# Kernel optimization log

Measured on AMD Instinct MI355X. Metric: run time of the kernel, lower is better.

## Reference

```python
import jax, jax.numpy as jnp
import numpy as np

# AlphaPose skeleton (directed, as used by the module) -------------------
_EDGES = [(0,5),(0,6),(1,2),(2,4),(1,3),(5,7),(7,9),(6,8),(8,10),(5,6),
          (5,11),(6,12),(11,12),(11,13),(13,15),(12,14),(14,16)]
_N = 17

def _gcn_norm_adj():
    # PyG GCNConv: add self-loops, deg from target (col), norm = d^-1/2[src]*d^-1/2[dst]
    A = np.zeros((_N, _N), dtype=np.float32)
    for s, t in _EDGES:
        A[t, s] = 1.0               # message flows source -> target
    A += np.eye(_N, dtype=np.float32)  # self loops
    deg = A.sum(axis=1)                # in-degree incl. self loop
    dinv = 1.0 / np.sqrt(deg)
    return (dinv[:, None] * A * dinv[None, :]).astype(np.float32)

A_HAT = jnp.asarray(_gcn_norm_adj())  # [17,17], A_hat[t,s]

B, T, F, H, LH, C = 256, 128, 2, 128, 256, 1


def setup_inputs() -> dict:
    key = jax.random.key(0)
    ks = jax.random.split(key, 8)
    s = 0.05
    return {
        "keypoints": jax.random.normal(ks[0], (B, T, _N, F), jnp.float32),
        "W1": jax.random.normal(ks[1], (F, H), jnp.float32) * s,
        "b1": jnp.zeros((H,), jnp.float32),
        "W2": jax.random.normal(ks[2], (H, H), jnp.float32) * s,
        "b2": jnp.zeros((H,), jnp.float32),
        "W_ih": jax.random.normal(ks[3], (4 * LH, H), jnp.float32) * s,
        "W_hh": jax.random.normal(ks[4], (4 * LH, LH), jnp.float32) * s,
        "b_ih": jnp.zeros((4 * LH,), jnp.float32),
        "b_hh": jnp.zeros((4 * LH,), jnp.float32),
        "W_fc": jax.random.normal(ks[5], (C, LH), jnp.float32) * s,
        "b_fc": jnp.zeros((C,), jnp.float32),
    }


def _lstm(x, W_ih, W_hh, b_ih, b_hh):
    # x: [B, T, H] -> hs: [B, T, LH]; PyTorch gate order i, f, g, o
    b, lh = x.shape[0], W_hh.shape[1]
    bias = b_ih + b_hh
    xw = jnp.einsum('bth,gh->btg', x, W_ih) + bias  # precompute input proj

    def step(carry, xt):
        h, c = carry
        z = xt + h @ W_hh.T
        i, f, g, o = jnp.split(z, 4, axis=-1)
        i, f, o = jax.nn.sigmoid(i), jax.nn.sigmoid(f), jax.nn.sigmoid(o)
        g = jnp.tanh(g)
        c = f * c + i * g
        h = o * jnp.tanh(c)
        return (h, c), h

    h0 = jnp.zeros((b, lh), x.dtype)
    _, hs = jax.lax.scan(step, (h0, h0), xw.transpose(1, 0, 2))
    return hs.transpose(1, 0, 2)


def reference(keypoints, W1, b1, W2, b2, W_ih, W_hh, b_ih, b_hh, W_fc, b_fc):
    # Batched GCNConv: out = A_hat @ (X W) + b, fused over all B*T frames
    x = jnp.einsum('nm,btmh->btnh', A_HAT, keypoints @ W1) + b1
    x = jax.nn.relu(x)
    x = jnp.einsum('nm,btmh->btnh', A_HAT, x @ W2) + b2
    x = jax.nn.relu(x)
    pooled = x.mean(axis=2)                      # global_mean_pool -> [B,T,H]
    hs = _lstm(pooled, W_ih, W_hh, b_ih, b_hh)   # [B,T,LH]
    feat = hs.max(axis=1)                        # max over time -> [B,LH]
    out = feat @ W_fc.T + b_fc                   # [B,1]
    return jax.nn.sigmoid(out).squeeze(1)        # [B]
```

## Files before the change

### kernel.cpp

```cpp
#include <hip/hip_runtime.h>
#include <hip/hip_bf16.h>
#include <math.h>

#define NNODE 17
#define HF    128
#define TT    128
#define BB    256
#define LHID  256
#define G4    1024
#define ZSTR  1032

typedef short short8 __attribute__((ext_vector_type(8)));
typedef float f32x4  __attribute__((ext_vector_type(4)));

#define OFF_AHAT   0
#define OFF_WIT    512
#define OFF_BIAS   (OFF_WIT + 131072)
#define OFF_WPK    (OFF_BIAS + 1024)
#define OFF_POOLED (OFF_WPK + 131072)
#define OFF_XW     (OFF_POOLED + 4194304)
#define OFF_FEAT   (OFF_XW + 33554432)

__device__ inline unsigned int f2bf(float x) {
    unsigned int u = __float_as_uint(x);
    return (u + 0x7fffu + ((u >> 16) & 1u)) >> 16;
}

__global__ __launch_bounds__(64) void prep_ahat_k(float* __restrict__ Ahat) {
    __shared__ float A[289];
    __shared__ float dinv[NNODE];
    const int t = threadIdx.x;
    for (int i = t; i < 289; i += 64) A[i] = 0.f;
    __syncthreads();
    if (t == 0) {
        const int es[17] = {0,0,1,2,1,5,7,6,8,5,5,6,11,11,13,12,14};
        const int et[17] = {5,6,2,4,3,7,9,8,10,6,11,12,12,13,15,14,16};
        for (int e = 0; e < 17; e++) A[et[e]*17 + es[e]] = 1.f;
        for (int n = 0; n < NNODE; n++) A[n*17 + n] += 1.f;
    }
    __syncthreads();
    if (t < NNODE) {
        float s = 0.f;
        for (int m = 0; m < NNODE; m++) s += A[t*17 + m];
        dinv[t] = rsqrtf(s);
    }
    __syncthreads();
    for (int i = t; i < 289; i += 64) {
        int n = i / 17, m = i % 17;
        Ahat[i] = dinv[n] * A[i] * dinv[m];
    }
}

__global__ __launch_bounds__(256) void prep_wt_k(
    const float* __restrict__ Wih,
    const float* __restrict__ bih, const float* __restrict__ bhh,
    float* __restrict__ WIT, float* __restrict__ bias_sum)
{
    const int k = blockIdx.x;
    const int g0 = threadIdx.x;
    for (int g = g0; g < G4; g += 256)
        WIT[(size_t)k*G4 + g] = Wih[(size_t)g*HF + k];
    if (k == 0)
        for (int g = g0; g < G4; g += 256)
            bias_sum[g] = bih[g] + bhh[g];
}

__global__ __launch_bounds__(256) void prep_pack_k(
    const float* __restrict__ Whh, unsigned short* __restrict__ Wpk)
{
    const int tid = blockIdx.x * 256 + threadIdx.x;
    const int lane = tid & 63;
    const int kc   = (tid >> 6) & 7;
    const int t    = (tid >> 9) & 7;
    const int w    = (tid >> 12) & 7;
    const int col  = w*128 + t*16 + (lane & 15);
    const int kb   = kc*32 + (lane >> 4)*8;
    const float4 v0 = *(const float4*)(Whh + (size_t)col*LHID + kb);
    const float4 v1 = *(const float4*)(Whh + (size_t)col*LHID + kb + 4);
    uint4 o;
    o.x = f2bf(v0.x) | (f2bf(v0.y) << 16);
    o.y = f2bf(v0.z) | (f2bf(v0.w) << 16);
    o.z = f2bf(v1.x) | (f2bf(v1.y) << 16);
    o.w = f2bf(v1.z) | (f2bf(v1.w) << 16);
    *(uint4*)(Wpk + (size_t)tid*8) = o;
}

__global__ __launch_bounds__(128) void gcn_pool_k(
    const float* __restrict__ kp, const float* __restrict__ W1,
    const float* __restrict__ b1, const float* __restrict__ W2,
    const float* __restrict__ b2, const float* __restrict__ Ahat,
    float* __restrict__ pooled)
{
    const int f = blockIdx.x;
    const int j = threadIdx.x;
    __shared__ float Ah[289];
    __shared__ float X[34];
    __shared__ float AhT[128][20];
    if (j < 34) X[j] = kp[(size_t)f*34 + j];
    for (int i = j; i < 289; i += 128) Ah[i] = Ahat[i];
    __syncthreads();
    float ax0[NNODE], ax1[NNODE];
    #pragma unroll
    for (int n = 0; n < NNODE; n++) {
        float s0 = 0.f, s1 = 0.f;
        #pragma unroll
        for (int m = 0; m < NNODE; m++) {
            float a = Ah[n*17 + m];
            s0 += a * X[2*m];
            s1 += a * X[2*m + 1];
        }
        ax0[n] = s0; ax1[n] = s1;
    }
    const float w10 = W1[j], w11 = W1[HF + j], bb1 = b1[j];
    float h1[NNODE];
    #pragma unroll
    for (int n = 0; n < NNODE; n++)
        h1[n] = fmaxf(fmaf(ax0[n], w10, fmaf(ax1[n], w11, bb1)), 0.f);
    float gcol[NNODE];
    #pragma unroll
    for (int n = 0; n < NNODE; n++) {
        float s = 0.f;
        #pragma unroll
        for (int m = 0; m < NNODE; m++) s += Ah[n*17 + m] * h1[m];
        gcol[n] = s;
    }
    #pragma unroll
    for (int n = 0; n < NNODE; n++) AhT[j][n] = gcol[n];
    __syncthreads();
    float acc[NNODE];
    #pragma unroll
    for (int n = 0; n < NNODE; n++) acc[n] = 0.f;
    for (int k = 0; k < HF; k++) {
        float w = W2[k*HF + j];
        #pragma unroll
        for (int n = 0; n < NNODE; n++) acc[n] = fmaf(AhT[k][n], w, acc[n]);
    }
    const float bb2 = b2[j];
    float s = 0.f;
    #pragma unroll
    for (int n = 0; n < NNODE; n++) s += fmaxf(acc[n] + bb2, 0.f);
    pooled[(size_t)f*HF + j] = s * (1.f/17.f);
}

__global__ __launch_bounds__(256) void xw_gemm_k(
    const float* __restrict__ pooled, const float* __restrict__ WIT,
    const float* __restrict__ bias_sum, float* __restrict__ xw)
{
    const int row0 = blockIdx.x * 16;
    const int col  = blockIdx.y * 256 + threadIdx.x;
    __shared__ float P[16][HF];
    #pragma unroll
    for (int i = 0; i < 8; i++) {
        int e = threadIdx.x + i*256;
        P[e >> 7][e & 127] = pooled[(size_t)(row0 + (e >> 7))*HF + (e & 127)];
    }
    __syncthreads();
    float acc[16];
    #pragma unroll
    for (int r = 0; r < 16; r++) acc[r] = 0.f;
    for (int k = 0; k < HF; k++) {
        float w = WIT[(size_t)k*G4 + col];
        #pragma unroll
        for (int r = 0; r < 16; r++) acc[r] = fmaf(P[r][k], w, acc[r]);
    }
    float bs = bias_sum[col];
    #pragma unroll
    for (int r = 0; r < 16; r++)
        xw[(size_t)(row0 + r)*G4 + col] = acc[r] + bs;
}

__global__ __launch_bounds__(1024, 4) void lstm_mfma_k(
    const float* __restrict__ xw, const unsigned short* __restrict__ Wpk,
    float* __restrict__ feat)
{
    const int b0  = blockIdx.x * 8;
    const int tid = threadIdx.x;
    const int w   = tid >> 6;
    const int l   = tid & 63;
    const int kh  = w >> 3;
    const int cg  = w & 7;
    const int row = tid >> 7;
    const int u0  = (tid & 127) * 2;

    __shared__ float zbuf[2][8][ZSTR];
    __shared__ unsigned short hpack[8][64][8];

    if (tid < 512) ((uint4*)hpack)[tid] = make_uint4(0u, 0u, 0u, 0u);

    float c0 = 0.f, c1 = 0.f;
    float hm0 = -1e30f, hm1 = -1e30f;
    const unsigned short* wb = Wpk + (size_t)cg*32768 + (size_t)kh*2048 + (size_t)l*8;
    const float* xb = xw + ((size_t)(b0 + row)*TT)*G4 + u0;
    const int zr = (l >> 4) * 4;
    const int zc = cg*128 + (l & 15);
    __syncthreads();

    for (int t = 0; t < TT; ++t) {
        float2 xg[4];
        #pragma unroll
        for (int g = 0; g < 4; ++g)
            xg[g] = *(const float2*)(xb + (size_t)t*G4 + g*256);

        short8 a[4];
        #pragma unroll
        for (int kc = 0; kc < 4; ++kc)
            a[kc] = *(const short8*)&hpack[kh*4 + kc][l][0];

        short8 bc[4], bn[4];
        #pragma unroll
        for (int kc = 0; kc < 4; ++kc)
            bc[kc] = *(const short8*)(wb + kc*512);
        for (int tt = 0; tt < 8; ++tt) {
            if (tt < 7) {
                #pragma unroll
                for (int kc = 0; kc < 4; ++kc)
                    bn[kc] = *(const short8*)(wb + (tt+1)*4096 + kc*512);
            }
            f32x4 acc = {0.f, 0.f, 0.f, 0.f};
            #pragma unroll
            for (int kc = 0; kc < 4; ++kc)
                acc = __builtin_amdgcn_mfma_f32_16x16x32_bf16(a[kc], bc[kc], acc, 0, 0, 0);
            if (l < 32) {
                #pragma unroll
                for (int r = 0; r < 4; ++r)
                    zbuf[kh][zr + r][tt*16 + zc] = acc[r];
            }
            #pragma unroll
            for (int kc = 0; kc < 4; ++kc) bc[kc] = bn[kc];
        }
        __syncthreads();

        float2 ziA = *(const float2*)&zbuf[0][row][0*256 + u0];
        float2 ziB = *(const float2*)&zbuf[1][row][0*256 + u0];
        float2 zfA = *(const float2*)&zbuf[0][row][1*256 + u0];
        float2 zfB = *(const float2*)&zbuf[1][row][1*256 + u0];
        float2 zgA = *(const float2*)&zbuf[0][row][2*256 + u0];
        float2 zgB = *(const float2*)&zbuf[1][row][2*256 + u0];
        float2 zoA = *(const float2*)&zbuf[0][row][3*256 + u0];
        float2 zoB = *(const float2*)&zbuf[1][row][3*256 + u0];
        float hval[2];
        #pragma unroll
        for (int q = 0; q < 2; ++q) {
            float vi = ((const float*)&ziA)[q] + ((const float*)&ziB)[q] + ((const float*)&xg[0])[q];
            float vf = ((const float*)&zfA)[q] + ((const float*)&zfB)[q] + ((const float*)&xg[1])[q];
            float vg = ((const float*)&zgA)[q] + ((const float*)&zgB)[q] + ((const float*)&xg[2])[q];
            float vo = ((const float*)&zoA)[q] + ((const float*)&zoB)[q] + ((const float*)&xg[3])[q];
            float ii = __builtin_amdgcn_rcpf(1.f + __expf(-vi));
            float ff = __builtin_amdgcn_rcpf(1.f + __expf(-vf));
            float gg = 1.f - 2.f * __builtin_amdgcn_rcpf(__expf(2.f*vg) + 1.f);
            float oo = 1.f / (1.f + __expf(-vo));
            float cc = (q == 0) ? c0 : c1;
            float cn = fmaf(ff, cc, ii * gg);
            if (q == 0) c0 = cn; else c1 = cn;
            float th = 1.f - 2.f * __builtin_amdgcn_rcpf(__expf(2.f*cn) + 1.f);
            float hh = oo * th;
            if (q == 0) hm0 = fmaxf(hm0, hh); else hm1 = fmaxf(hm1, hh);
            hval[q] = hh;
        }
        unsigned int hp = f2bf(hval[0]) | (f2bf(hval[1]) << 16);
        *(unsigned int*)&hpack[u0 >> 5][((u0 >> 3) & 3)*16 + row][u0 & 7] = hp;
        __syncthreads();
    }
    *(float2*)(feat + (size_t)(b0 + row)*LHID + u0) = make_float2(hm0, hm1);
}

__global__ __launch_bounds__(64) void final_k(
    const float* __restrict__ feat, const float* __restrict__ Wfc,
    const float* __restrict__ bfc, float* __restrict__ out)
{
    const int b = blockIdx.x * 64 + threadIdx.x;
    float s = bfc[0];
    for (int u = 0; u < LHID; u++)
        s = fmaf(feat[(size_t)b*LHID + u], Wfc[u], s);
    out[b] = 1.f / (1.f + __expf(-s));
}

extern "C" void kernel_launch(void* const* d_in, const int* in_sizes, int n_in,
                              void* d_out, int out_size, void* d_ws, size_t ws_size,
                              hipStream_t stream) {
    const float* kp  = (const float*)d_in[0];
    const float* W1  = (const float*)d_in[1];
    const float* b1  = (const float*)d_in[2];
    const float* W2  = (const float*)d_in[3];
    const float* b2  = (const float*)d_in[4];
    const float* Wih = (const float*)d_in[5];
    const float* Whh = (const float*)d_in[6];
    const float* bih = (const float*)d_in[7];
    const float* bhh = (const float*)d_in[8];
    const float* Wfc = (const float*)d_in[9];
    const float* bfc = (const float*)d_in[10];

    float* ws     = (float*)d_ws;
    float* Ahat   = ws + OFF_AHAT;
    float* WIT    = ws + OFF_WIT;
    float* bias   = ws + OFF_BIAS;
    unsigned short* Wpk = (unsigned short*)(ws + OFF_WPK);
    float* pooled = ws + OFF_POOLED;
    float* xw     = ws + OFF_XW;
    float* feat   = ws + OFF_FEAT;
    float* out    = (float*)d_out;

    hipLaunchKernelGGL(prep_ahat_k, dim3(1), dim3(64), 0, stream, Ahat);
    hipLaunchKernelGGL(prep_wt_k, dim3(128), dim3(256), 0, stream,
                       Wih, bih, bhh, WIT, bias);
    hipLaunchKernelGGL(prep_pack_k, dim3(128), dim3(256), 0, stream, Whh, Wpk);
    hipLaunchKernelGGL(gcn_pool_k, dim3(BB*TT), dim3(128), 0, stream,
                       kp, W1, b1, W2, b2, Ahat, pooled);
    hipLaunchKernelGGL(xw_gemm_k, dim3(BB*TT/16, 4), dim3(256), 0, stream,
                       pooled, WIT, bias, xw);
    hipLaunchKernelGGL(lstm_mfma_k, dim3(BB/8), dim3(1024), 0, stream, xw, Wpk, feat);
    hipLaunchKernelGGL(final_k, dim3(4), dim3(64), 0, stream, feat, Wfc, bfc, out);
}
```

Measured before the change: 1.601 ms.

## Keep W_hh resident in registers across LSTM timesteps and drop K-split

Each wave now loads its 4x8 short8 slice of the packed W_hh once before the time loop and keeps it in registers. Previously those weights were re-streamed from global memory on every one of the 128 steps. The K dimension is no longer split across two wave halves, so each wave runs the full 8-chunk MFMA reduction for 4 column tiles. This removes the second zbuf partial-sum buffer and the extra adds. The cost is much higher register pressure (128 VGPRs for weights alone) with launch bounds of 1024 threads, so spills are possible.

```diff
diff --git a/kernel.cpp b/kernel.cpp
--- a/kernel.cpp
+++ b/kernel.cpp
@@ -177,22 +177,27 @@
     const int tid = threadIdx.x;
     const int w   = tid >> 6;
     const int l   = tid & 63;
-    const int kh  = w >> 3;
-    const int cg  = w & 7;
     const int row = tid >> 7;
     const int u0  = (tid & 127) * 2;
 
-    __shared__ float zbuf[2][8][ZSTR];
+    __shared__ float zbuf[8][ZSTR];
     __shared__ unsigned short hpack[8][64][8];
 
     if (tid < 512) ((uint4*)hpack)[tid] = make_uint4(0u, 0u, 0u, 0u);
+
+    const unsigned short* wb = Wpk + (size_t)(w >> 1)*32768 + (size_t)(w & 1)*16384 + (size_t)l*8;
+    short8 wreg[4][8];
+    #pragma unroll
+    for (int tt = 0; tt < 4; ++tt)
+        #pragma unroll
+        for (int kc = 0; kc < 8; ++kc)
+            wreg[tt][kc] = *(const short8*)(wb + tt*4096 + kc*512);
 
     float c0 = 0.f, c1 = 0.f;
     float hm0 = -1e30f, hm1 = -1e30f;
-    const unsigned short* wb = Wpk + (size_t)cg*32768 + (size_t)kh*2048 + (size_t)l*8;
     const float* xb = xw + ((size_t)(b0 + row)*TT)*G4 + u0;
-    const int zr = (l >> 4) * 4;
-    const int zc = cg*128 + (l & 15);
+    const int zr  = (l >> 4) * 4;
+    const int zc0 = (w >> 1)*128 + (w & 1)*64 + (l & 15);
     __syncthreads();
 
     for (int t = 0; t < TT; ++t) {
@@ -201,50 +206,36 @@
         for (int g = 0; g < 4; ++g)
             xg[g] = *(const float2*)(xb + (size_t)t*G4 + g*256);
 
-        short8 a[4];
-        #pragma unroll
-        for (int kc = 0; kc < 4; ++kc)
-            a[kc] = *(const short8*)&hpack[kh*4 + kc][l][0];
-
-        short8 bc[4], bn[4];
-        #pragma unroll
-        for (int kc = 0; kc < 4; ++kc)
-            bc[kc] = *(const short8*)(wb + kc*512);
-        for (int tt = 0; tt < 8; ++tt) {
-            if (tt < 7) {
-                #pragma unroll
-                for (int kc = 0; kc < 4; ++kc)
-                    bn[kc] = *(const short8*)(wb + (tt+1)*4096 + kc*512);
-            }
+        short8 a[8];
+        #pragma unroll
+        for (int kc = 0; kc < 8; ++kc)
+            a[kc] = *(const short8*)&hpack[kc][l][0];
+
+        #pragma unroll
+        for (int tt = 0; tt < 4; ++tt) {
             f32x4 acc = {0.f, 0.f, 0.f, 0.f};
             #pragma unroll
-            for (int kc = 0; kc < 4; ++kc)
-                acc = __builtin_amdgcn_mfma_f32_16x16x32_bf16(a[kc], bc[kc], acc, 0, 0, 0);
+            for (int kc = 0; kc < 8; ++kc)
+                acc = __builtin_amdgcn_mfma_f32_16x16x32_bf16(a[kc], wreg[tt][kc], acc, 0, 0, 0);
             if (l < 32) {
                 #pragma unroll
                 for (int r = 0; r < 4; ++r)
-                    zbuf[kh][zr + r][tt*16 + zc] = acc[r];
+                    zbuf[zr + r][tt*16 + zc0] = acc[r];
             }
-            #pragma unroll
-            for (int kc = 0; kc < 4; ++kc) bc[kc] = bn[kc];
         }
         __syncthreads();
 
-        float2 ziA = *(const float2*)&zbuf[0][row][0*256 + u0];
-        float2 ziB = *(const float2*)&zbuf[1][row][0*256 + u0];
-        float2 zfA = *(const float2*)&zbuf[0][row][1*256 + u0];
-        float2 zfB = *(const float2*)&zbuf[1][row][1*256 + u0];
-        float2 zgA = *(const float2*)&zbuf[0][row][2*256 + u0];
-        float2 zgB = *(const float2*)&zbuf[1][row][2*256 + u0];
-        float2 zoA = *(const float2*)&zbuf[0][row][3*256 + u0];
-        float2 zoB = *(const float2*)&zbuf[1][row][3*256 + u0];
+        float2 zi = *(const float2*)&zbuf[row][0*256 + u0];
+        float2 zf = *(const float2*)&zbuf[row][1*256 + u0];
+        float2 zg = *(const float2*)&zbuf[row][2*256 + u0];
+        float2 zo = *(const float2*)&zbuf[row][3*256 + u0];
         float hval[2];
         #pragma unroll
         for (int q = 0; q < 2; ++q) {
-            float vi = ((const float*)&ziA)[q] + ((const float*)&ziB)[q] + ((const float*)&xg[0])[q];
-            float vf = ((const float*)&zfA)[q] + ((const float*)&zfB)[q] + ((const float*)&xg[1])[q];
-            float vg = ((const float*)&zgA)[q] + ((const float*)&zgB)[q] + ((const float*)&xg[2])[q];
-            float vo = ((const float*)&zoA)[q] + ((const float*)&zoB)[q] + ((const float*)&xg[3])[q];
+            float vi = ((const float*)&zi)[q] + ((const float*)&xg[0])[q];
+            float vf = ((const float*)&zf)[q] + ((const float*)&xg[1])[q];
+            float vg = ((const float*)&zg)[q] + ((const float*)&xg[2])[q];
+            float vo = ((const float*)&zo)[q] + ((const float*)&xg[3])[q];
             float ii = __builtin_amdgcn_rcpf(1.f + __expf(-vi));
             float ff = __builtin_amdgcn_rcpf(1.f + __expf(-vf));
             float gg = 1.f - 2.f * __builtin_amdgcn_rcpf(__expf(2.f*vg) + 1.f);
```

Result: slower. 1.825 ms (+14.0%).
